# Kernel optimization log

Measured on AMD Instinct MI355X. Metric: run time of the kernel, lower is better.

## Reference

```python
import jax, jax.numpy as jnp
import numpy as np

N = 50000   # nodes
E = 800000  # edges
F = 128     # num_node_features
H = 256     # hidden_channels
C = 40      # num_classes


def setup_inputs() -> dict:
    key = jax.random.key(0)
    ks = jax.random.split(key, 8)
    x = jax.random.normal(ks[0], (N, F), dtype=jnp.float32)
    edge_index = jax.random.randint(ks[1], (2, E), 0, N, dtype=jnp.int32)
    # GCNConv linear weights (PyG: lin has no bias; bias added post-aggregation)
    W1 = jax.random.normal(ks[2], (H, F), dtype=jnp.float32) * (1.0 / np.sqrt(F))
    b1 = jnp.zeros((H,), dtype=jnp.float32)
    W2 = jax.random.normal(ks[3], (H, H), dtype=jnp.float32) * (1.0 / np.sqrt(H))
    b2 = jnp.zeros((H,), dtype=jnp.float32)
    Wout = jax.random.normal(ks[4], (C, H), dtype=jnp.float32) * (1.0 / np.sqrt(H))
    bout = jnp.zeros((C,), dtype=jnp.float32)
    return {"x": x, "edge_index": edge_index,
            "W1": W1, "b1": b1, "W2": W2, "b2": b2,
            "Wout": Wout, "bout": bout}


def gcn_conv(x, src, dst, W, b, n):
    """PyG GCNConv: sym-normalized aggregation with self-loops.
    deg computed as in-degree on dst (gcn_norm), +1 for self loop.
    """
    h = x @ W.T  # [n, out]
    ones = jnp.ones((src.shape[0],), dtype=h.dtype)
    deg = jax.ops.segment_sum(ones, dst, num_segments=n) + 1.0  # self loop
    dinv = jax.lax.rsqrt(deg)  # deg >= 1, safe
    norm = dinv[src] * dinv[dst]                 # [E]
    agg = jax.ops.segment_sum(norm[:, None] * h[src], dst, num_segments=n)
    agg = agg + (dinv * dinv)[:, None] * h       # self-loop term
    return agg + b


def reference(x, edge_index, W1, b1, W2, b2, Wout, bout):
    src, dst = edge_index[0], edge_index[1]
    h = jax.nn.relu(gcn_conv(x, src, dst, W1, b1, N))
    h = gcn_conv(h, src, dst, W2, b2, N)
    return h @ Wout.T + bout  # [N, C] logits
```

## Files before the change

kernel.cpp:

```cpp
#include <hip/hip_runtime.h>

#define N_NODES 50000
#define N_EDGES 800000
#define F_IN    128
#define H_DIM   256
#define C_OUT   40
#define MT_TOT  (N_NODES / 16)
#define TPAD    64
#define NBIN1   196
#define NCHB    200
#define CHSZ    (N_EDGES / NCHB)
#define CVT_X   (N_NODES * F_IN / 4)
#define CVT_W1B (H_DIM * F_IN / 4 / 256)

typedef unsigned short u16;
typedef unsigned int   u32;
typedef short bf16x8 __attribute__((ext_vector_type(8)));
typedef float f32x4  __attribute__((ext_vector_type(4)));

__device__ inline float bfbits2f(u16 u) { return __uint_as_float(((u32)u) << 16); }
__device__ inline u16 f2bf(float f) {
    u32 u = __float_as_uint(f);
    u += 0x7fffu + ((u >> 16) & 1u);
    return (u16)(u >> 16);
}
__device__ inline u32 pack2(float a, float b) {
    return (u32)f2bf(a) | ((u32)f2bf(b) << 16);
}

__global__ __launch_bounds__(256) void pre_k(const int* __restrict__ dst, int* __restrict__ Ht,
                                             const float4* __restrict__ W1, uint2* __restrict__ W1b,
                                             const float* __restrict__ W2, const float* __restrict__ Wo,
                                             const float* __restrict__ b2, const float* __restrict__ bo,
                                             u16* __restrict__ Wcb, float* __restrict__ bc) {
    __shared__ int hist[NBIN1];
    __shared__ float red[256];
    const int t = threadIdx.x;
    if (blockIdx.x < NCHB) {
        const int b = blockIdx.x;
        if (t < NBIN1) hist[t] = 0;
        __syncthreads();
        for (int i = b * CHSZ + t; i < (b + 1) * CHSZ; i += 256)
            atomicAdd(&hist[dst[i] >> 8], 1);
        __syncthreads();
        if (t < NBIN1) Ht[t * NCHB + b] = hist[t];
        return;
    }
    if (blockIdx.x < NCHB + CVT_W1B) {
        int i = (blockIdx.x - NCHB) * 256 + t;
        float4 v = W1[i];
        uint2 o; o.x = pack2(v.x, v.y); o.y = pack2(v.z, v.w);
        W1b[i] = o;
        return;
    }
    const int c = blockIdx.x - NCHB - CVT_W1B;
    float acc = 0.f;
    for (int o = 0; o < H_DIM; o += 8) {
        float w2v[8];
#pragma unroll
        for (int j = 0; j < 8; j++) w2v[j] = W2[(size_t)(o + j) * H_DIM + t];
#pragma unroll
        for (int j = 0; j < 8; j++) acc += Wo[(size_t)c * H_DIM + o + j] * w2v[j];
    }
    Wcb[(size_t)c * H_DIM + t] = f2bf(acc);
    red[t] = b2[t] * Wo[(size_t)c * H_DIM + t];
    __syncthreads();
    for (int off = 128; off > 0; off >>= 1) {
        if (t < off) red[t] += red[t + off];
        __syncthreads();
    }
    if (t == 0) bc[c] = red[0] + bo[c];
}

__global__ __launch_bounds__(256) void p1scan_k(int* __restrict__ Ht, int* __restrict__ totals) {
    __shared__ int sc[256];
    const int t = threadIdx.x;
    const int g = blockIdx.x;
    int v = (t < NCHB) ? Ht[g * NCHB + t] : 0;
    sc[t] = v;
    __syncthreads();
    for (int off = 1; off < 256; off <<= 1) {
        int u = (t >= off) ? sc[t - off] : 0;
        __syncthreads();
        sc[t] += u;
        __syncthreads();
    }
    if (t < NCHB) Ht[g * NCHB + t] = sc[t] - v;
    if (t == NCHB - 1) totals[g] = sc[t];
}

__global__ __launch_bounds__(256) void p1base_k(const int* __restrict__ totals,
                                                int* __restrict__ base, int* __restrict__ rowptr) {
    __shared__ int sc[256];
    const int t = threadIdx.x;
    int v = (t < NBIN1) ? totals[t] : 0;
    sc[t] = v;
    __syncthreads();
    for (int off = 1; off < 256; off <<= 1) {
        int u = (t >= off) ? sc[t - off] : 0;
        __syncthreads();
        sc[t] += u;
        __syncthreads();
    }
    if (t < NBIN1) base[t] = sc[t] - v;
    if (t == NBIN1 - 1) base[NBIN1] = sc[t];
    if (t == 0) rowptr[N_NODES] = N_EDGES;
}

__global__ __launch_bounds__(256) void p2scatter_k(const int* __restrict__ src, const int* __restrict__ dst,
                                                   const int* __restrict__ Ht, const int* __restrict__ base,
                                                   uint2* __restrict__ T) {
    __shared__ int cur[NBIN1];
    const int t = threadIdx.x;
    const int b = blockIdx.x;
    if (t < NBIN1) cur[t] = base[t] + Ht[t * NCHB + b];
    __syncthreads();
    for (int i = b * CHSZ + t; i < (b + 1) * CHSZ; i += 256) {
        const int s = src[i], d = dst[i];
        const int pos = atomicAdd(&cur[d >> 8], 1);
        uint2 ed; ed.x = (u32)s; ed.y = (u32)d;
        T[pos] = ed;
    }
}

__global__ __launch_bounds__(256) void p3_k(const uint2* __restrict__ T, const int* __restrict__ base,
                                            int* __restrict__ rowptr, float* __restrict__ dinv,
                                            u32* __restrict__ edata) {
    __shared__ int hcnt[256];
    __shared__ int sc[256];
    __shared__ int cur[256];
    const int t = threadIdx.x;
    const int g = blockIdx.x;
    const int nbeg = base[g], nend = base[g + 1];
    hcnt[t] = 0;
    __syncthreads();
    for (int i = nbeg + t; i < nend; i += 256)
        atomicAdd(&hcnt[T[i].y & 255], 1);
    __syncthreads();
    const int my = hcnt[t];
    sc[t] = my;
    __syncthreads();
    for (int off = 1; off < 256; off <<= 1) {
        int u = (t >= off) ? sc[t - off] : 0;
        __syncthreads();
        sc[t] += u;
        __syncthreads();
    }
    const int rbeg = nbeg + sc[t] - my;
    const int node = g * 256 + t;
    if (node < N_NODES) {
        rowptr[node] = rbeg;
        dinv[node] = rsqrtf((float)my + 1.0f);
    }
    cur[t] = rbeg;
    __syncthreads();
    for (int i = nbeg + t; i < nend; i += 256) {
        const uint2 e = T[i];
        const int pos = atomicAdd(&cur[e.y & 255], 1);
        edata[pos] = e.x;
    }
}

__global__ __launch_bounds__(256) void xcvt_k(const float4* __restrict__ x,
                                              const float* __restrict__ dinv,
                                              uint2* __restrict__ xb) {
    int i = blockIdx.x * 256 + threadIdx.x;
    if (i >= CVT_X) return;
    const int row = i >> 5;
    const float s = dinv[row];
    float4 v = x[i];
    uint2 o; o.x = pack2(s * v.x, s * v.y); o.y = pack2(s * v.z, s * v.w);
    xb[i] = o;
}

__global__ __launch_bounds__(256) void gather1_k(const u32* __restrict__ xb,
                                                 const int* __restrict__ rowptr,
                                                 const u32* __restrict__ edata,
                                                 const float* __restrict__ dinv,
                                                 u32* __restrict__ aggx) {
    const int node = __builtin_amdgcn_readfirstlane(blockIdx.x * 4 + (threadIdx.x >> 6));
    const int lane = threadIdx.x & 63;
    if (node >= N_NODES) return;
    const int beg = __builtin_amdgcn_readfirstlane(rowptr[node]);
    const int end = __builtin_amdgcn_readfirstlane(rowptr[node + 1]);
    const float dd = dinv[node];
    const u32 vs = xb[(size_t)node * 64 + lane];
    float a0 = bfbits2f((u16)vs);
    float a1 = bfbits2f((u16)(vs >> 16));
    int e = beg;
    for (; e + 7 < end; e += 8) {
        u32 s8[8];
#pragma unroll
        for (int j = 0; j < 8; j++) s8[j] = edata[e + j];
        u32 v[8];
#pragma unroll
        for (int j = 0; j < 8; j++) v[j] = xb[(size_t)s8[j] * 64 + lane];
#pragma unroll
        for (int j = 0; j < 8; j++) {
            a0 += bfbits2f((u16)v[j]);
            a1 += bfbits2f((u16)(v[j] >> 16));
        }
    }
    for (; e < end; e++) {
        const u32 v0 = xb[(size_t)edata[e] * 64 + lane];
        a0 += bfbits2f((u16)v0);
        a1 += bfbits2f((u16)(v0 >> 16));
    }
    aggx[(size_t)node * 64 + lane] = pack2(dd * a0, dd * a1);
}

__global__ __launch_bounds__(256) void bgemm1f_k(const u16* __restrict__ X,
                                                 const u16* __restrict__ W1b,
                                                 const float* __restrict__ b1,
                                                 const u16* __restrict__ Wcb,
                                                 const float* __restrict__ dinv,
                                                 u16* __restrict__ tb) {
    constexpr int KF1 = F_IN / 32;
    constexpr int KF2 = H_DIM / 32;
    __shared__ __align__(16) u16 hs[2][16][H_DIM + 8];
    const int wave = threadIdx.x >> 6;
    const int lane = threadIdx.x & 63;
    const int quad = lane >> 4;
    const int nn = lane & 15;
    const int ngbase = wave * 64;

    bf16x8 Bf[4][KF1];
    float bb[4];
#pragma unroll
    for (int j = 0; j < 4; j++) {
        const int wr = ngbase + j * 16 + nn;
#pragma unroll
        for (int kf = 0; kf < KF1; kf++)
            Bf[j][kf] = *(const bf16x8*)(W1b + (size_t)wr * F_IN + kf * 32 + quad * 8);
        bb[j] = b1[wr];
    }
    bf16x8 Bh[KF2];
    {
        int hr = wave * 16 + nn;
        if (hr > C_OUT - 1) hr = C_OUT - 1;
#pragma unroll
        for (int kf = 0; kf < KF2; kf++)
            Bh[kf] = *(const bf16x8*)(Wcb + (size_t)hr * H_DIM + kf * 32 + quad * 8);
    }

    int mt = blockIdx.x;
    if (mt >= MT_TOT) return;
    const int stride = gridDim.x;
    int buf = 0;

    bf16x8 Acur[KF1], Anext[KF1];
    {
        const u16* ap = X + (size_t)(mt * 16 + nn) * F_IN + quad * 8;
#pragma unroll
        for (int kf = 0; kf < KF1; kf++) Acur[kf] = *(const bf16x8*)(ap + kf * 32);
    }

    while (true) {
        const int mtn = mt + stride;
        if (mtn < MT_TOT) {
            const u16* ap = X + (size_t)(mtn * 16 + nn) * F_IN + quad * 8;
#pragma unroll
            for (int kf = 0; kf < KF1; kf++) Anext[kf] = *(const bf16x8*)(ap + kf * 32);
        }

        f32x4 acc[4];
#pragma unroll
        for (int j = 0; j < 4; j++) acc[j] = (f32x4){0.f, 0.f, 0.f, 0.f};
#pragma unroll
        for (int kf = 0; kf < KF1; kf++)
#pragma unroll
            for (int j = 0; j < 4; j++)
                acc[j] = __builtin_amdgcn_mfma_f32_16x16x32_bf16(Acur[kf], Bf[j][kf], acc[j], 0, 0, 0);

#pragma unroll
        for (int j = 0; j < 4; j++)
#pragma unroll
            for (int r = 0; r < 4; r++)
                hs[buf][quad * 4 + r][ngbase + j * 16 + nn] = f2bf(fmaxf(acc[j][r] + bb[j], 0.f));
        __syncthreads();

        if (wave < 3) {
            f32x4 ah = (f32x4){0.f, 0.f, 0.f, 0.f};
#pragma unroll
            for (int kf = 0; kf < KF2; kf++) {
                bf16x8 af = *(const bf16x8*)(&hs[buf][nn][kf * 32 + quad * 8]);
                ah = __builtin_amdgcn_mfma_f32_16x16x32_bf16(af, Bh[kf], ah, 0, 0, 0);
            }
            const int col = wave * 16 + nn;
#pragma unroll
            for (int r = 0; r < 4; r++) {
                const int row = mt * 16 + quad * 4 + r;
                tb[(size_t)row * TPAD + col] = f2bf(dinv[row] * ah[r]);
            }
        }

        if (mtn >= MT_TOT) break;
#pragma unroll
        for (int kf = 0; kf < KF1; kf++) Acur[kf] = Anext[kf];
        mt = mtn;
        buf ^= 1;
    }
}

__global__ __launch_bounds__(256) void gatherO_k(const u32* __restrict__ tb,
                                                 const int* __restrict__ rowptr,
                                                 const u32* __restrict__ edata,
                                                 const float* __restrict__ dinv,
                                                 const float* __restrict__ bc,
                                                 float* __restrict__ out) {
    const int node = __builtin_amdgcn_readfirstlane(blockIdx.x * 4 + (threadIdx.x >> 6));
    const int lane = threadIdx.x & 63;
    if (node >= N_NODES) return;
    const int lc = lane & 31;
    const int beg = __builtin_amdgcn_readfirstlane(rowptr[node]);
    const int end = __builtin_amdgcn_readfirstlane(rowptr[node + 1]);
    const float dd = dinv[node];
    const u32 vs = tb[(size_t)node * (TPAD / 2) + lc];
    float a0 = bfbits2f((u16)vs);
    float a1 = bfbits2f((u16)(vs >> 16));
    int e = beg;
    for (; e + 7 < end; e += 8) {
        u32 s8[8];
#pragma unroll
        for (int j = 0; j < 8; j++) s8[j] = edata[e + j];
        u32 v[8];
#pragma unroll
        for (int j = 0; j < 8; j++) v[j] = tb[(size_t)s8[j] * (TPAD / 2) + lc];
#pragma unroll
        for (int j = 0; j < 8; j++) {
            a0 += bfbits2f((u16)v[j]);
            a1 += bfbits2f((u16)(v[j] >> 16));
        }
    }
    for (; e < end; e++) {
        const u32 v0 = tb[(size_t)edata[e] * (TPAD / 2) + lc];
        a0 += bfbits2f((u16)v0);
        a1 += bfbits2f((u16)(v0 >> 16));
    }
    if (lane < C_OUT / 2) {
        float2 o;
        o.x = dd * a0 + bc[2 * lane];
        o.y = dd * a1 + bc[2 * lane + 1];
        *(float2*)(out + (size_t)node * C_OUT + 2 * lane) = o;
    }
}

extern "C" void kernel_launch(void* const* d_in, const int* in_sizes, int n_in,
                              void* d_out, int out_size, void* d_ws, size_t ws_size,
                              hipStream_t stream) {
    const float* x    = (const float*)d_in[0];
    const int*   ei   = (const int*)d_in[1];
    const float* W1   = (const float*)d_in[2];
    const float* b1   = (const float*)d_in[3];
    const float* W2   = (const float*)d_in[4];
    const float* b2   = (const float*)d_in[5];
    const float* Wout = (const float*)d_in[6];
    const float* bout = (const float*)d_in[7];
    float* out = (float*)d_out;

    const int* src = ei;
    const int* dst = ei + N_EDGES;

    char* ws = (char*)d_ws;
    size_t o = 0;
    auto alloc = [&](size_t bytes) { size_t p = o; o = (o + bytes + 255) & ~(size_t)255; return p; };
    int*   Ht     = (int*)(ws + alloc((size_t)NBIN1 * NCHB * 4));
    int*   totals = (int*)(ws + alloc((size_t)NBIN1 * 4));
    int*   base   = (int*)(ws + alloc((size_t)(NBIN1 + 1) * 4));
    float* dinv   = (float*)(ws + alloc((size_t)N_NODES * 4));
    int*   rowptr = (int*)(ws + alloc((size_t)(N_NODES + 1) * 4));
    uint2* T      = (uint2*)(ws + alloc((size_t)N_EDGES * 8));
    u32*   edata  = (u32*)(ws + alloc((size_t)N_EDGES * 4));
    u16*   xb     = (u16*)(ws + alloc((size_t)N_NODES * F_IN * 2));
    u16*   aggxb  = (u16*)(ws + alloc((size_t)N_NODES * F_IN * 2));
    u16*   tb     = (u16*)(ws + alloc((size_t)N_NODES * TPAD * 2));
    u16*   W1b    = (u16*)(ws + alloc((size_t)H_DIM * F_IN * 2));
    u16*   Wcb    = (u16*)(ws + alloc((size_t)C_OUT * H_DIM * 2));
    float* bc     = (float*)(ws + alloc((size_t)C_OUT * 4));

    pre_k<<<NCHB + CVT_W1B + C_OUT, 256, 0, stream>>>(
        dst, Ht, (const float4*)W1, (uint2*)W1b, W2, Wout, b2, bout, Wcb, bc);
    p1scan_k<<<NBIN1, 256, 0, stream>>>(Ht, totals);
    p1base_k<<<1, 256, 0, stream>>>(totals, base, rowptr);
    p2scatter_k<<<NCHB, 256, 0, stream>>>(src, dst, Ht, base, T);
    p3_k<<<NBIN1, 256, 0, stream>>>(T, base, rowptr, dinv, edata);
    xcvt_k<<<(CVT_X + 255) / 256, 256, 0, stream>>>((const float4*)x, dinv, (uint2*)xb);

    gather1_k<<<(N_NODES + 3) / 4, 256, 0, stream>>>((const u32*)xb, rowptr, edata, dinv, (u32*)aggxb);
    bgemm1f_k<<<768, 256, 0, stream>>>(aggxb, W1b, b1, Wcb, dinv, tb);
    gatherO_k<<<(N_NODES + 3) / 4, 256, 0, stream>>>((const u32*)tb, rowptr, edata, dinv, bc, out);
}
```

Before: 198.9 us.

## Fuse scan kernels via last-block atomic, fold x conversion into CSR pass, shrink tb

Merges the two scan kernels into one, where the last block to finish, detected with an atomic counter, computes the global bin bases. Folds the bf16 conversion of x into the per-bin CSR kernel, which reuses its per-node dinv from shared memory, so one launch is dropped. Shrinks the padded tb buffer from 64 to 40 columns, which cuts gather traffic in the output stage. The cost is atomic counter synchronisation, fewer blocks (196) doing the x conversion, and 20-lane loads that are less aligned.

New measurement: 196.8 us. About the same (-1.1%).

```diff
diff --git a/kernel.cpp b/kernel.cpp
--- a/kernel.cpp
+++ b/kernel.cpp
@@ -6,7 +6,6 @@
 #define H_DIM   256
 #define C_OUT   40
 #define MT_TOT  (N_NODES / 16)
-#define TPAD    64
 #define NBIN1   196
 #define NCHB    200
 #define CHSZ    (N_EDGES / NCHB)
@@ -32,12 +31,14 @@
                                              const float4* __restrict__ W1, uint2* __restrict__ W1b,
                                              const float* __restrict__ W2, const float* __restrict__ Wo,
                                              const float* __restrict__ b2, const float* __restrict__ bo,
-                                             u16* __restrict__ Wcb, float* __restrict__ bc) {
+                                             u16* __restrict__ Wcb, float* __restrict__ bc,
+                                             int* __restrict__ done) {
     __shared__ int hist[NBIN1];
     __shared__ float red[256];
     const int t = threadIdx.x;
     if (blockIdx.x < NCHB) {
         const int b = blockIdx.x;
+        if (b == 0 && t == 0) *done = 0;
         if (t < NBIN1) hist[t] = 0;
         __syncthreads();
         for (int i = b * CHSZ + t; i < (b + 1) * CHSZ; i += 256)
@@ -72,8 +73,11 @@
     if (t == 0) bc[c] = red[0] + bo[c];
 }
 
-__global__ __launch_bounds__(256) void p1scan_k(int* __restrict__ Ht, int* __restrict__ totals) {
+__global__ __launch_bounds__(256) void scan_k(int* __restrict__ Ht, int* __restrict__ totals,
+                                              int* __restrict__ base, int* __restrict__ rowptr,
+                                              int* __restrict__ done) {
     __shared__ int sc[256];
+    __shared__ int lastflag;
     const int t = threadIdx.x;
     const int g = blockIdx.x;
     int v = (t < NCHB) ? Ht[g * NCHB + t] : 0;
@@ -86,15 +90,17 @@
         __syncthreads();
     }
     if (t < NCHB) Ht[g * NCHB + t] = sc[t] - v;
-    if (t == NCHB - 1) totals[g] = sc[t];
-}
-
-__global__ __launch_bounds__(256) void p1base_k(const int* __restrict__ totals,
-                                                int* __restrict__ base, int* __restrict__ rowptr) {
-    __shared__ int sc[256];
-    const int t = threadIdx.x;
-    int v = (t < NBIN1) ? totals[t] : 0;
-    sc[t] = v;
+    if (t == NCHB - 1)
+        __hip_atomic_store(&totals[g], sc[t], __ATOMIC_RELAXED, __HIP_MEMORY_SCOPE_AGENT);
+    __syncthreads();
+    if (t == 0) {
+        int old = __hip_atomic_fetch_add(done, 1, __ATOMIC_ACQ_REL, __HIP_MEMORY_SCOPE_AGENT);
+        lastflag = (old == NBIN1 - 1);
+    }
+    __syncthreads();
+    if (!lastflag) return;
+    int tv = (t < NBIN1) ? __hip_atomic_load(&totals[t], __ATOMIC_RELAXED, __HIP_MEMORY_SCOPE_AGENT) : 0;
+    sc[t] = tv;
     __syncthreads();
     for (int off = 1; off < 256; off <<= 1) {
         int u = (t >= off) ? sc[t - off] : 0;
@@ -102,7 +108,7 @@
         sc[t] += u;
         __syncthreads();
     }
-    if (t < NBIN1) base[t] = sc[t] - v;
+    if (t < NBIN1) base[t] = sc[t] - tv;
     if (t == NBIN1 - 1) base[NBIN1] = sc[t];
     if (t == 0) rowptr[N_NODES] = N_EDGES;
 }
@@ -123,12 +129,14 @@
     }
 }
 
-__global__ __launch_bounds__(256) void p3_k(const uint2* __restrict__ T, const int* __restrict__ base,
-                                            int* __restrict__ rowptr, float* __restrict__ dinv,
-                                            u32* __restrict__ edata) {
+__global__ __launch_bounds__(256) void p3x_k(const uint2* __restrict__ T, const int* __restrict__ base,
+                                             int* __restrict__ rowptr, float* __restrict__ dinv,
+                                             u32* __restrict__ edata,
+                                             const float4* __restrict__ x, uint2* __restrict__ xb) {
     __shared__ int hcnt[256];
     __shared__ int sc[256];
     __shared__ int cur[256];
+    __shared__ float sdinv[256];
     const int t = threadIdx.x;
     const int g = blockIdx.x;
     const int nbeg = base[g], nend = base[g + 1];
@@ -148,9 +156,11 @@
     }
     const int rbeg = nbeg + sc[t] - my;
     const int node = g * 256 + t;
+    const float dv = rsqrtf((float)my + 1.0f);
+    sdinv[t] = dv;
     if (node < N_NODES) {
         rowptr[node] = rbeg;
-        dinv[node] = rsqrtf((float)my + 1.0f);
+        dinv[node] = dv;
     }
     cur[t] = rbeg;
     __syncthreads();
@@ -159,18 +169,15 @@
         const int pos = atomicAdd(&cur[e.y & 255], 1);
         edata[pos] = e.x;
     }
-}
-
-__global__ __launch_bounds__(256) void xcvt_k(const float4* __restrict__ x,
-                                              const float* __restrict__ dinv,
-                                              uint2* __restrict__ xb) {
-    int i = blockIdx.x * 256 + threadIdx.x;
-    if (i >= CVT_X) return;
-    const int row = i >> 5;
-    const float s = dinv[row];
-    float4 v = x[i];
-    uint2 o; o.x = pack2(s * v.x, s * v.y); o.y = pack2(s * v.z, s * v.w);
-    xb[i] = o;
+    const int gbase = g * 256 * (F_IN / 4);
+    for (int i = t; i < 256 * (F_IN / 4); i += 256) {
+        const int gi = gbase + i;
+        if (gi >= CVT_X) break;
+        const float s = sdinv[i >> 5];
+        float4 v = x[gi];
+        uint2 o; o.x = pack2(s * v.x, s * v.y); o.y = pack2(s * v.z, s * v.w);
+        xb[gi] = o;
+    }
 }
 
 __global__ __launch_bounds__(256) void gather1_k(const u32* __restrict__ xb,
@@ -287,10 +294,12 @@
                 ah = __builtin_amdgcn_mfma_f32_16x16x32_bf16(af, Bh[kf], ah, 0, 0, 0);
             }
             const int col = wave * 16 + nn;
-#pragma unroll
-            for (int r = 0; r < 4; r++) {
-                const int row = mt * 16 + quad * 4 + r;
-                tb[(size_t)row * TPAD + col] = f2bf(dinv[row] * ah[r]);
+            if (col < C_OUT) {
+#pragma unroll
+                for (int r = 0; r < 4; r++) {
+                    const int row = mt * 16 + quad * 4 + r;
+                    tb[(size_t)row * C_OUT + col] = f2bf(dinv[row] * ah[r]);
+                }
             }
         }
 
@@ -312,10 +321,11 @@
     const int lane = threadIdx.x & 63;
     if (node >= N_NODES) return;
     const int lc = lane & 31;
+    const bool act = (lc < C_OUT / 2);
     const int beg = __builtin_amdgcn_readfirstlane(rowptr[node]);
     const int end = __builtin_amdgcn_readfirstlane(rowptr[node + 1]);
     const float dd = dinv[node];
-    const u32 vs = tb[(size_t)node * (TPAD / 2) + lc];
+    const u32 vs = act ? tb[(size_t)node * (C_OUT / 2) + lc] : 0u;
     float a0 = bfbits2f((u16)vs);
     float a1 = bfbits2f((u16)(vs >> 16));
     int e = beg;
@@ -325,7 +335,7 @@
         for (int j = 0; j < 8; j++) s8[j] = edata[e + j];
         u32 v[8];
 #pragma unroll
-        for (int j = 0; j < 8; j++) v[j] = tb[(size_t)s8[j] * (TPAD / 2) + lc];
+        for (int j = 0; j < 8; j++) v[j] = act ? tb[(size_t)s8[j] * (C_OUT / 2) + lc] : 0u;
 #pragma unroll
         for (int j = 0; j < 8; j++) {
             a0 += bfbits2f((u16)v[j]);
@@ -333,7 +343,7 @@
         }
     }
     for (; e < end; e++) {
-        const u32 v0 = tb[(size_t)edata[e] * (TPAD / 2) + lc];
+        const u32 v0 = act ? tb[(size_t)edata[e] * (C_OUT / 2) + lc] : 0u;
         a0 += bfbits2f((u16)v0);
         a1 += bfbits2f((u16)(v0 >> 16));
     }
@@ -373,18 +383,17 @@
     u32*   edata  = (u32*)(ws + alloc((size_t)N_EDGES * 4));
     u16*   xb     = (u16*)(ws + alloc((size_t)N_NODES * F_IN * 2));
     u16*   aggxb  = (u16*)(ws + alloc((size_t)N_NODES * F_IN * 2));
-    u16*   tb     = (u16*)(ws + alloc((size_t)N_NODES * TPAD * 2));
+    u16*   tb     = (u16*)(ws + alloc((size_t)N_NODES * C_OUT * 2 + 256));
     u16*   W1b    = (u16*)(ws + alloc((size_t)H_DIM * F_IN * 2));
     u16*   Wcb    = (u16*)(ws + alloc((size_t)C_OUT * H_DIM * 2));
     float* bc     = (float*)(ws + alloc((size_t)C_OUT * 4));
+    int*   done   = (int*)(ws + alloc(256));
 
     pre_k<<<NCHB + CVT_W1B + C_OUT, 256, 0, stream>>>(
-        dst, Ht, (const float4*)W1, (uint2*)W1b, W2, Wout, b2, bout, Wcb, bc);
-    p1scan_k<<<NBIN1, 256, 0, stream>>>(Ht, totals);
-    p1base_k<<<1, 256, 0, stream>>>(totals, base, rowptr);
+        dst, Ht, (const float4*)W1, (uint2*)W1b, W2, Wout, b2, bout, Wcb, bc, done);
+    scan_k<<<NBIN1, 256, 0, stream>>>(Ht, totals, base, rowptr, done);
     p2scatter_k<<<NCHB, 256, 0, stream>>>(src, dst, Ht, base, T);
-    p3_k<<<NBIN1, 256, 0, stream>>>(T, base, rowptr, dinv, edata);
-    xcvt_k<<<(CVT_X + 255) / 256, 256, 0, stream>>>((const float4*)x, dinv, (uint2*)xb);
+    p3x_k<<<NBIN1, 256, 0, stream>>>(T, base, rowptr, dinv, edata, (const float4*)x, (uint2*)xb);
 
     gather1_k<<<(N_NODES + 3) / 4, 256, 0, stream>>>((const u32*)xb, rowptr, edata, dinv, (u32*)aggxb);
     bgemm1f_k<<<768, 256, 0, stream>>>(aggxb, W1b, b1, Wcb, dinv, tb);
```

## Build CSR with global atomics and fuse x conversion into edge scatter

Applied to the files above, without the earlier changes.

Replaces the two-level binned CSR construction (histogram, two scans, scatter into temp, per-bin local sort) with a direct global-atomic degree count, a single-pass block scan that takes its base offset from an atomic counter, and a global-atomic scatter of source ids. Row ends come from the post-scatter cursors, so rows need not sit in node order. The x bf16 conversion now runs in the same launch as the scatter, and the output projection buffer shrinks from a padded width of 64 to 40 columns. The aim is to cut kernel launches and temporary edge traffic. In exchange it adds contended global atomics and makes the edge order inside each row nondeterministic.

New measurement: 242.2 us. 21.8% more time.

```diff
diff --git a/kernel.cpp b/kernel.cpp
--- a/kernel.cpp
+++ b/kernel.cpp
@@ -6,11 +6,11 @@
 #define H_DIM   256
 #define C_OUT   40
 #define MT_TOT  (N_NODES / 16)
-#define TPAD    64
-#define NBIN1   196
-#define NCHB    200
-#define CHSZ    (N_EDGES / NCHB)
+#define HB      400
+#define ECH     (N_EDGES / HB)
+#define SCB     ((N_NODES + 255) / 256)
 #define CVT_X   (N_NODES * F_IN / 4)
+#define XVB     ((CVT_X + 255) / 256)
 #define CVT_W1B (H_DIM * F_IN / 4 / 256)
 
 typedef unsigned short u16;
@@ -28,32 +28,27 @@
     return (u32)f2bf(a) | ((u32)f2bf(b) << 16);
 }
 
-__global__ __launch_bounds__(256) void pre_k(const int* __restrict__ dst, int* __restrict__ Ht,
+__global__ __launch_bounds__(256) void pre_k(const int* __restrict__ dst, int* __restrict__ deg,
                                              const float4* __restrict__ W1, uint2* __restrict__ W1b,
                                              const float* __restrict__ W2, const float* __restrict__ Wo,
                                              const float* __restrict__ b2, const float* __restrict__ bo,
                                              u16* __restrict__ Wcb, float* __restrict__ bc) {
-    __shared__ int hist[NBIN1];
     __shared__ float red[256];
     const int t = threadIdx.x;
-    if (blockIdx.x < NCHB) {
+    if (blockIdx.x < HB) {
         const int b = blockIdx.x;
-        if (t < NBIN1) hist[t] = 0;
-        __syncthreads();
-        for (int i = b * CHSZ + t; i < (b + 1) * CHSZ; i += 256)
-            atomicAdd(&hist[dst[i] >> 8], 1);
-        __syncthreads();
-        if (t < NBIN1) Ht[t * NCHB + b] = hist[t];
+        for (int i = b * ECH + t; i < (b + 1) * ECH; i += 256)
+            atomicAdd(&deg[dst[i]], 1);
         return;
     }
-    if (blockIdx.x < NCHB + CVT_W1B) {
-        int i = (blockIdx.x - NCHB) * 256 + t;
+    if (blockIdx.x < HB + CVT_W1B) {
+        int i = (blockIdx.x - HB) * 256 + t;
         float4 v = W1[i];
         uint2 o; o.x = pack2(v.x, v.y); o.y = pack2(v.z, v.w);
-        W1b[i] = o;
+        ((uint2*)W1b)[i] = o;
         return;
     }
-    const int c = blockIdx.x - NCHB - CVT_W1B;
+    const int c = blockIdx.x - HB - CVT_W1B;
     float acc = 0.f;
     for (int o = 0; o < H_DIM; o += 8) {
         float w2v[8];
@@ -72,12 +67,15 @@
     if (t == 0) bc[c] = red[0] + bo[c];
 }
 
-__global__ __launch_bounds__(256) void p1scan_k(int* __restrict__ Ht, int* __restrict__ totals) {
+__global__ __launch_bounds__(256) void scan_k(const int* __restrict__ deg, int* __restrict__ rowptr,
+                                              int* __restrict__ cur, float* __restrict__ dinv,
+                                              int* __restrict__ gctr) {
     __shared__ int sc[256];
+    __shared__ int sbase;
     const int t = threadIdx.x;
-    const int g = blockIdx.x;
-    int v = (t < NCHB) ? Ht[g * NCHB + t] : 0;
-    sc[t] = v;
+    const int node = blockIdx.x * 256 + t;
+    const int d = (node < N_NODES) ? deg[node] : 0;
+    sc[t] = d;
     __syncthreads();
     for (int off = 1; off < 256; off <<= 1) {
         int u = (t >= off) ? sc[t - off] : 0;
@@ -85,86 +83,32 @@
         sc[t] += u;
         __syncthreads();
     }
-    if (t < NCHB) Ht[g * NCHB + t] = sc[t] - v;
-    if (t == NCHB - 1) totals[g] = sc[t];
-}
-
-__global__ __launch_bounds__(256) void p1base_k(const int* __restrict__ totals,
-                                                int* __restrict__ base, int* __restrict__ rowptr) {
-    __shared__ int sc[256];
+    if (t == 255) sbase = atomicAdd(gctr, sc[255]);
+    __syncthreads();
+    if (node < N_NODES) {
+        const int rb = sbase + sc[t] - d;
+        rowptr[node] = rb;
+        cur[node]    = rb;
+        dinv[node]   = rsqrtf((float)d + 1.0f);
+    }
+}
+
+__global__ __launch_bounds__(256) void scatx_k(const int* __restrict__ src, const int* __restrict__ dst,
+                                               int* __restrict__ cur, u32* __restrict__ edata,
+                                               const float4* __restrict__ x,
+                                               const float* __restrict__ dinv,
+                                               uint2* __restrict__ xb) {
     const int t = threadIdx.x;
-    int v = (t < NBIN1) ? totals[t] : 0;
-    sc[t] = v;
-    __syncthreads();
-    for (int off = 1; off < 256; off <<= 1) {
-        int u = (t >= off) ? sc[t - off] : 0;
-        __syncthreads();
-        sc[t] += u;
-        __syncthreads();
-    }
-    if (t < NBIN1) base[t] = sc[t] - v;
-    if (t == NBIN1 - 1) base[NBIN1] = sc[t];
-    if (t == 0) rowptr[N_NODES] = N_EDGES;
-}
-
-__global__ __launch_bounds__(256) void p2scatter_k(const int* __restrict__ src, const int* __restrict__ dst,
-                                                   const int* __restrict__ Ht, const int* __restrict__ base,
-                                                   uint2* __restrict__ T) {
-    __shared__ int cur[NBIN1];
-    const int t = threadIdx.x;
-    const int b = blockIdx.x;
-    if (t < NBIN1) cur[t] = base[t] + Ht[t * NCHB + b];
-    __syncthreads();
-    for (int i = b * CHSZ + t; i < (b + 1) * CHSZ; i += 256) {
-        const int s = src[i], d = dst[i];
-        const int pos = atomicAdd(&cur[d >> 8], 1);
-        uint2 ed; ed.x = (u32)s; ed.y = (u32)d;
-        T[pos] = ed;
-    }
-}
-
-__global__ __launch_bounds__(256) void p3_k(const uint2* __restrict__ T, const int* __restrict__ base,
-                                            int* __restrict__ rowptr, float* __restrict__ dinv,
-                                            u32* __restrict__ edata) {
-    __shared__ int hcnt[256];
-    __shared__ int sc[256];
-    __shared__ int cur[256];
-    const int t = threadIdx.x;
-    const int g = blockIdx.x;
-    const int nbeg = base[g], nend = base[g + 1];
-    hcnt[t] = 0;
-    __syncthreads();
-    for (int i = nbeg + t; i < nend; i += 256)
-        atomicAdd(&hcnt[T[i].y & 255], 1);
-    __syncthreads();
-    const int my = hcnt[t];
-    sc[t] = my;
-    __syncthreads();
-    for (int off = 1; off < 256; off <<= 1) {
-        int u = (t >= off) ? sc[t - off] : 0;
-        __syncthreads();
-        sc[t] += u;
-        __syncthreads();
-    }
-    const int rbeg = nbeg + sc[t] - my;
-    const int node = g * 256 + t;
-    if (node < N_NODES) {
-        rowptr[node] = rbeg;
-        dinv[node] = rsqrtf((float)my + 1.0f);
-    }
-    cur[t] = rbeg;
-    __syncthreads();
-    for (int i = nbeg + t; i < nend; i += 256) {
-        const uint2 e = T[i];
-        const int pos = atomicAdd(&cur[e.y & 255], 1);
-        edata[pos] = e.x;
-    }
-}
-
-__global__ __launch_bounds__(256) void xcvt_k(const float4* __restrict__ x,
-                                              const float* __restrict__ dinv,
-                                              uint2* __restrict__ xb) {
-    int i = blockIdx.x * 256 + threadIdx.x;
+    if (blockIdx.x < HB) {
+        const int b = blockIdx.x;
+        for (int i = b * ECH + t; i < (b + 1) * ECH; i += 256) {
+            const int s = src[i], d = dst[i];
+            const int pos = atomicAdd(&cur[d], 1);
+            edata[pos] = (u32)s;
+        }
+        return;
+    }
+    const int i = (blockIdx.x - HB) * 256 + t;
     if (i >= CVT_X) return;
     const int row = i >> 5;
     const float s = dinv[row];
@@ -175,6 +119,7 @@
 
 __global__ __launch_bounds__(256) void gather1_k(const u32* __restrict__ xb,
                                                  const int* __restrict__ rowptr,
+                                                 const int* __restrict__ cur,
                                                  const u32* __restrict__ edata,
                                                  const float* __restrict__ dinv,
                                                  u32* __restrict__ aggx) {
@@ -182,7 +127,7 @@
     const int lane = threadIdx.x & 63;
     if (node >= N_NODES) return;
     const int beg = __builtin_amdgcn_readfirstlane(rowptr[node]);
-    const int end = __builtin_amdgcn_readfirstlane(rowptr[node + 1]);
+    const int end = __builtin_amdgcn_readfirstlane(cur[node]);
     const float dd = dinv[node];
     const u32 vs = xb[(size_t)node * 64 + lane];
     float a0 = bfbits2f((u16)vs);
@@ -287,10 +232,12 @@
                 ah = __builtin_amdgcn_mfma_f32_16x16x32_bf16(af, Bh[kf], ah, 0, 0, 0);
             }
             const int col = wave * 16 + nn;
-#pragma unroll
-            for (int r = 0; r < 4; r++) {
-                const int row = mt * 16 + quad * 4 + r;
-                tb[(size_t)row * TPAD + col] = f2bf(dinv[row] * ah[r]);
+            if (col < C_OUT) {
+#pragma unroll
+                for (int r = 0; r < 4; r++) {
+                    const int row = mt * 16 + quad * 4 + r;
+                    tb[(size_t)row * C_OUT + col] = f2bf(dinv[row] * ah[r]);
+                }
             }
         }
 
@@ -304,6 +251,7 @@
 
 __global__ __launch_bounds__(256) void gatherO_k(const u32* __restrict__ tb,
                                                  const int* __restrict__ rowptr,
+                                                 const int* __restrict__ cur,
                                                  const u32* __restrict__ edata,
                                                  const float* __restrict__ dinv,
                                                  const float* __restrict__ bc,
@@ -312,10 +260,11 @@
     const int lane = threadIdx.x & 63;
     if (node >= N_NODES) return;
     const int lc = lane & 31;
+    const bool act = (lc < C_OUT / 2);
     const int beg = __builtin_amdgcn_readfirstlane(rowptr[node]);
-    const int end = __builtin_amdgcn_readfirstlane(rowptr[node + 1]);
+    const int end = __builtin_amdgcn_readfirstlane(cur[node]);
     const float dd = dinv[node];
-    const u32 vs = tb[(size_t)node * (TPAD / 2) + lc];
+    const u32 vs = act ? tb[(size_t)node * (C_OUT / 2) + lc] : 0u;
     float a0 = bfbits2f((u16)vs);
     float a1 = bfbits2f((u16)(vs >> 16));
     int e = beg;
@@ -325,7 +274,7 @@
         for (int j = 0; j < 8; j++) s8[j] = edata[e + j];
         u32 v[8];
 #pragma unroll
-        for (int j = 0; j < 8; j++) v[j] = tb[(size_t)s8[j] * (TPAD / 2) + lc];
+        for (int j = 0; j < 8; j++) v[j] = act ? tb[(size_t)s8[j] * (C_OUT / 2) + lc] : 0u;
 #pragma unroll
         for (int j = 0; j < 8; j++) {
             a0 += bfbits2f((u16)v[j]);
@@ -333,7 +282,7 @@
         }
     }
     for (; e < end; e++) {
-        const u32 v0 = tb[(size_t)edata[e] * (TPAD / 2) + lc];
+        const u32 v0 = act ? tb[(size_t)edata[e] * (C_OUT / 2) + lc] : 0u;
         a0 += bfbits2f((u16)v0);
         a1 += bfbits2f((u16)(v0 >> 16));
     }
@@ -364,29 +313,27 @@
     char* ws = (char*)d_ws;
     size_t o = 0;
     auto alloc = [&](size_t bytes) { size_t p = o; o = (o + bytes + 255) & ~(size_t)255; return p; };
-    int*   Ht     = (int*)(ws + alloc((size_t)NBIN1 * NCHB * 4));
-    int*   totals = (int*)(ws + alloc((size_t)NBIN1 * 4));
-    int*   base   = (int*)(ws + alloc((size_t)(NBIN1 + 1) * 4));
+    int*   zeroed = (int*)(ws + alloc((size_t)(N_NODES + 1) * 4));
+    int*   deg    = zeroed;
+    int*   gctr   = zeroed + N_NODES;
     float* dinv   = (float*)(ws + alloc((size_t)N_NODES * 4));
-    int*   rowptr = (int*)(ws + alloc((size_t)(N_NODES + 1) * 4));
-    uint2* T      = (uint2*)(ws + alloc((size_t)N_EDGES * 8));
+    int*   rowptr = (int*)(ws + alloc((size_t)N_NODES * 4));
+    int*   cur    = (int*)(ws + alloc((size_t)N_NODES * 4));
     u32*   edata  = (u32*)(ws + alloc((size_t)N_EDGES * 4));
     u16*   xb     = (u16*)(ws + alloc((size_t)N_NODES * F_IN * 2));
     u16*   aggxb  = (u16*)(ws + alloc((size_t)N_NODES * F_IN * 2));
-    u16*   tb     = (u16*)(ws + alloc((size_t)N_NODES * TPAD * 2));
+    u16*   tb     = (u16*)(ws + alloc((size_t)N_NODES * C_OUT * 2 + 256));
     u16*   W1b    = (u16*)(ws + alloc((size_t)H_DIM * F_IN * 2));
     u16*   Wcb    = (u16*)(ws + alloc((size_t)C_OUT * H_DIM * 2));
     float* bc     = (float*)(ws + alloc((size_t)C_OUT * 4));
 
-    pre_k<<<NCHB + CVT_W1B + C_OUT, 256, 0, stream>>>(
-        dst, Ht, (const float4*)W1, (uint2*)W1b, W2, Wout, b2, bout, Wcb, bc);
-    p1scan_k<<<NBIN1, 256, 0, stream>>>(Ht, totals);
-    p1base_k<<<1, 256, 0, stream>>>(totals, base, rowptr);
-    p2scatter_k<<<NCHB, 256, 0, stream>>>(src, dst, Ht, base, T);
-    p3_k<<<NBIN1, 256, 0, stream>>>(T, base, rowptr, dinv, edata);
-    xcvt_k<<<(CVT_X + 255) / 256, 256, 0, stream>>>((const float4*)x, dinv, (uint2*)xb);
-
-    gather1_k<<<(N_NODES + 3) / 4, 256, 0, stream>>>((const u32*)xb, rowptr, edata, dinv, (u32*)aggxb);
+    hipMemsetAsync(zeroed, 0, (size_t)(N_NODES + 1) * 4, stream);
+    pre_k<<<HB + CVT_W1B + C_OUT, 256, 0, stream>>>(
+        dst, deg, (const float4*)W1, (uint2*)W1b, W2, Wout, b2, bout, Wcb, bc);
+    scan_k<<<SCB, 256, 0, stream>>>(deg, rowptr, cur, dinv, gctr);
+    scatx_k<<<HB + XVB, 256, 0, stream>>>(src, dst, cur, edata, (const float4*)x, dinv, (uint2*)xb);
+
+    gather1_k<<<(N_NODES + 3) / 4, 256, 0, stream>>>((const u32*)xb, rowptr, cur, edata, dinv, (u32*)aggxb);
     bgemm1f_k<<<768, 256, 0, stream>>>(aggxb, W1b, b1, Wcb, dinv, tb);
-    gatherO_k<<<(N_NODES + 3) / 4, 256, 0, stream>>>((const u32*)tb, rowptr, edata, dinv, bc, out);
-}
+    gatherO_k<<<(N_NODES + 3) / 4, 256, 0, stream>>>((const u32*)tb, rowptr, cur, edata, dinv, bc, out);
+}
```
